# Kernel tuning notes

Hardware: AMD Instinct MI355X
Metric: run time of the kernel (lower is better)

## Reference

```python
import jax, jax.numpy as jnp
import numpy as np

B, S, H, N_HEAD = 2, 2048, 1024, 16
NEG = float(-(2 ** 32) + 1)  # -4294967295.0, the module's padding value
EPS = 1e-08


def setup_inputs() -> dict:
    key = jax.random.key(0)
    ks = jax.random.split(key, 11)
    sc = 0.02
    return {
        "queries": jax.random.normal(ks[0], (B, S, H), dtype=jnp.float32),
        "keys": jax.random.normal(ks[1], (B, S, H), dtype=jnp.float32),
        "values": jax.random.normal(ks[2], (B, S, H), dtype=jnp.float32),
        "Wq": jax.random.normal(ks[3], (H, H), dtype=jnp.float32) * sc,
        "bq": jax.random.normal(ks[4], (H,), dtype=jnp.float32) * sc,
        "Wk": jax.random.normal(ks[5], (H, H), dtype=jnp.float32) * sc,
        "bk": jax.random.normal(ks[6], (H,), dtype=jnp.float32) * sc,
        "Wv": jax.random.normal(ks[7], (H, H), dtype=jnp.float32) * sc,
        "bv": jax.random.normal(ks[8], (H,), dtype=jnp.float32) * sc,
        "Wo": jax.random.normal(ks[9], (H, H), dtype=jnp.float32) * sc,
        "bo": jax.random.normal(ks[10], (H,), dtype=jnp.float32) * sc,
    }


def reference(queries, keys, values, Wq, bq, Wk, bk, Wv, bv, Wo, bo):
    n = N_HEAD
    Bb, Sq, Hh = queries.shape
    Sk = keys.shape[1]
    d = Hh // n

    # Linear + ReLU projections
    Q = jax.nn.relu(queries @ Wq + bq)  # [B,Sq,H]
    K = jax.nn.relu(keys @ Wk + bk)     # [B,Sk,H]
    V = jax.nn.relu(values @ Wv + bv)   # [B,Sk,H]

    # chunk(dim=2) + cat(dim=0) == head-major split: [n,B,S,d]
    Q_ = Q.reshape(Bb, Sq, n, d).transpose(2, 0, 1, 3)
    K_ = K.reshape(Bb, Sk, n, d).transpose(2, 0, 1, 3)
    V_ = V.reshape(Bb, Sk, n, d).transpose(2, 0, 1, 3)

    # key padding mask from full (pre-chunk) K: [B,Sk]
    key_masks = jnp.sign(jnp.abs(jnp.sum(K, axis=-1)))

    # scores: [n,B,Sq,Sk], scaled by sqrt(per-head dim)
    scores = jnp.einsum("hbqd,hbkd->hbqk", Q_, K_) / (d ** 0.5)

    # multiplicative padding-mask selection -> equivalent where()
    scores = jnp.where(key_masks[None, :, None, :] == 0.0, NEG, scores)

    # causal tril mask (masked=True)
    tril = jnp.tril(jnp.ones((Sq, Sk), dtype=scores.dtype))
    scores = jnp.where(tril[None, None] == 0.0, NEG, scores)

    attn = jax.nn.softmax(scores, axis=-1)
    out = jnp.einsum("hbqk,hbkd->hbqd", attn, V_)  # [n,B,Sq,d]

    # cat chunks back along feature dim: [B,Sq,H]
    out = out.transpose(1, 2, 0, 3).reshape(Bb, Sq, Hh)

    out = jax.nn.relu(out @ Wo + bo)
    # sublayer connection (dropout treated as identity for determinism)
    out = queries + out

    # layer norm with torch-style unbiased std, gamma=1, beta=0
    mean = out.mean(axis=-1, keepdims=True)
    std = jnp.std(out, axis=-1, ddof=1, keepdims=True)
    return (out - mean) / (std + EPS)
```

## Files before the change

kernel.cpp:

```cpp
#include <hip/hip_runtime.h>
#include <math.h>

typedef __bf16 bf16;
typedef __attribute__((ext_vector_type(8))) __bf16 bf16x8;
typedef __attribute__((ext_vector_type(4))) __bf16 bf16x4;
typedef __attribute__((ext_vector_type(4))) float f32x4;

typedef __attribute__((address_space(1))) unsigned int glb_u32;
typedef __attribute__((address_space(3))) unsigned int lds_u32;

#define NEGV (-4294967295.0f)
#define SCL2 0.18033688011112042f

__device__ __forceinline__ void async_cp16(const void* g, void* l) {
  __builtin_amdgcn_global_load_lds((glb_u32*)g, (lds_u32*)l, 16, 0, 0);
}

template <int CTRL>
__device__ __forceinline__ float dppf(float x) {
  return __builtin_bit_cast(float,
      __builtin_amdgcn_mov_dpp(__builtin_bit_cast(int, x), CTRL, 0xF, 0xF, true));
}
__device__ __forceinline__ float dpp_max16(float x) {
  x = fmaxf(x, dppf<0xB1>(x));
  x = fmaxf(x, dppf<0x4E>(x));
  x = fmaxf(x, dppf<0x141>(x));
  x = fmaxf(x, dppf<0x140>(x));
  return x;
}

__global__ __launch_bounds__(256) void wt_kernel(
    const float* __restrict__ W0, const float* __restrict__ W1,
    const float* __restrict__ W2, const float* __restrict__ W3,
    short* T0, short* T1, short* T2, short* T3) {
  __shared__ float tile[64][65];
  const float* W = blockIdx.z == 0 ? W0 : (blockIdx.z == 1 ? W1 : (blockIdx.z == 2 ? W2 : W3));
  bf16* T = (bf16*)(blockIdx.z == 0 ? T0 : (blockIdx.z == 1 ? T1 : (blockIdx.z == 2 ? T2 : T3)));
  const int k0 = blockIdx.y * 64, n0 = blockIdx.x * 64;
  const int tid = threadIdx.x;
  const int c = tid & 63, rr = tid >> 6;
#pragma unroll
  for (int i = 0; i < 16; i++) {
    int r = i * 4 + rr;
    tile[r][c] = W[(size_t)(k0 + r) * 1024 + n0 + c];
  }
  __syncthreads();
#pragma unroll
  for (int i = 0; i < 16; i++) {
    int r = i * 4 + rr;
    T[(size_t)(n0 + r) * 1024 + k0 + c] = (bf16)tile[c][r];
  }
}

__global__ __launch_bounds__(256) void qkv_gemm(
    const float* __restrict__ Xq, const float* __restrict__ Xk,
    const float* __restrict__ Xv,
    const short* Wtq_, const short* Wtk_, const short* Wtv_,
    const float* __restrict__ bq_, const float* __restrict__ bk_, const float* __restrict__ bv_,
    short* Qo_, short* Ko_, short* Vto_) {
  __shared__ float Af[128][32];
  __shared__ bf16 Blds[128][32];
  const int which = blockIdx.z;
  const float* X = which == 0 ? Xq : (which == 1 ? Xk : Xv);
  const bf16* Wt = (const bf16*)(which == 0 ? Wtq_ : (which == 1 ? Wtk_ : Wtv_));
  const float* bias = which == 0 ? bq_ : (which == 1 ? bk_ : bv_);
  const int m0 = blockIdx.y * 128, n0 = blockIdx.x * 128;
  const int tid = threadIdx.x, wid = tid >> 6, lane = tid & 63;
  const int wr = wid >> 1, wc = wid & 1;
  const int l15 = lane & 15, lg = lane >> 4;
  const f32x4 vzero = {0.f, 0.f, 0.f, 0.f};
  f32x4 acc[4][4];
#pragma unroll
  for (int m = 0; m < 4; m++)
#pragma unroll
    for (int n = 0; n < 4; n++) acc[m][n] = vzero;

  const int asrow = lane >> 3;
  const int acbs = ((lane & 7) * 16) ^ ((asrow & 7) << 4);
  const int bsr = wid * 32 + (lane >> 2);
  const int bscb = (lane & 3) * 16;

  for (int kt = 0; kt < 32; ++kt) {
#pragma unroll
    for (int c = 0; c < 4; c++) {
      const char* ga = (const char*)(X + (size_t)(m0 + wid * 32 + c * 8 + asrow) * 1024 + kt * 32) + acbs;
      async_cp16(ga, &Af[wid * 32 + c * 8][0]);
    }
    const char* gb = (const char*)(Wt + (size_t)(n0 + bsr) * 1024 + kt * 32) + bscb;
    async_cp16(gb, &Blds[wid * 32][0]);
    async_cp16(gb + 16 * 2048, &Blds[wid * 32 + 16][0]);
    __syncthreads();
    bf16x8 a[4], bb[4];
#pragma unroll
    for (int m = 0; m < 4; m++) {
      const int row = wr * 64 + m * 16 + l15;
      const int swz = (row & 7) << 4;
      const char* ar = (const char*)&Af[0][0] + row * 128;
      const float4 f0 = *(const float4*)(ar + ((lg * 32) ^ swz));
      const float4 f1 = *(const float4*)(ar + ((lg * 32 + 16) ^ swz));
      a[m][0] = (bf16)f0.x; a[m][1] = (bf16)f0.y; a[m][2] = (bf16)f0.z; a[m][3] = (bf16)f0.w;
      a[m][4] = (bf16)f1.x; a[m][5] = (bf16)f1.y; a[m][6] = (bf16)f1.z; a[m][7] = (bf16)f1.w;
    }
#pragma unroll
    for (int n = 0; n < 4; n++) bb[n] = *(const bf16x8*)&Blds[wc * 64 + n * 16 + l15][lg * 8];
#pragma unroll
    for (int m = 0; m < 4; m++)
#pragma unroll
      for (int n = 0; n < 4; n++)
        acc[m][n] = __builtin_amdgcn_mfma_f32_16x16x32_bf16(a[m], bb[n], acc[m][n], 0, 0, 0);
    __syncthreads();
  }

  if (which != 2) {
    bf16* Y = (bf16*)(which == 0 ? Qo_ : Ko_);
    const float osc = (which == 0) ? SCL2 : 1.0f;
#pragma unroll
    for (int n = 0; n < 4; n++) {
      const int col = n0 + wc * 64 + n * 16 + l15;
      const float bv = bias[col];
#pragma unroll
      for (int m = 0; m < 4; m++) {
        const int row0 = m0 + wr * 64 + m * 16 + lg * 4;
#pragma unroll
        for (int r = 0; r < 4; r++) {
          float v = acc[m][n][r] + bv;
          v = v > 0.f ? v : 0.f;
          Y[(size_t)(row0 + r) * 1024 + col] = (bf16)(v * osc);
        }
      }
    }
  } else {
    bf16* Vt = (bf16*)Vto_;
#pragma unroll
    for (int n = 0; n < 4; n++) {
      const int col = n0 + wc * 64 + n * 16 + l15;
      const float bv = bias[col];
#pragma unroll
      for (int m = 0; m < 4; m++) {
        const int row0 = m0 + wr * 64 + m * 16 + lg * 4;
        const int bb2 = row0 >> 11;
        const int s2 = row0 & 2047;
        bf16x4 pk;
#pragma unroll
        for (int r = 0; r < 4; r++) {
          float v = acc[m][n][r] + bv;
          v = v > 0.f ? v : 0.f;
          pk[r] = (bf16)v;
        }
        *(bf16x4*)(Vt + ((size_t)bb2 * 1024 + col) * 2048 + s2) = pk;
      }
    }
  }
}

__global__ __launch_bounds__(256) void out_gemm(
    const short* A_, const short* Wt_, const float* __restrict__ bias,
    short* __restrict__ Y_) {
  __shared__ bf16 Alds[128][32];
  __shared__ bf16 Blds[128][32];
  const bf16* X = (const bf16*)A_;
  const bf16* Wt = (const bf16*)Wt_;
  bf16* Y = (bf16*)Y_;
  const int m0 = blockIdx.y * 128, n0 = blockIdx.x * 128;
  const int tid = threadIdx.x, wid = tid >> 6, lane = tid & 63;
  const int wr = wid >> 1, wc = wid & 1;
  const int l15 = lane & 15, lg = lane >> 4;
  const f32x4 vzero = {0.f, 0.f, 0.f, 0.f};
  f32x4 acc[4][4];
#pragma unroll
  for (int m = 0; m < 4; m++)
#pragma unroll
    for (int n = 0; n < 4; n++) acc[m][n] = vzero;

  const int sr = wid * 32 + (lane >> 2);
  const int scb = (lane & 3) * 16;

  for (int kt = 0; kt < 32; ++kt) {
    const char* ga = (const char*)(X + (size_t)(m0 + sr) * 1024 + kt * 32) + scb;
    async_cp16(ga, &Alds[wid * 32][0]);
    async_cp16(ga + 16 * 2048, &Alds[wid * 32 + 16][0]);
    const char* gb = (const char*)(Wt + (size_t)(n0 + sr) * 1024 + kt * 32) + scb;
    async_cp16(gb, &Blds[wid * 32][0]);
    async_cp16(gb + 16 * 2048, &Blds[wid * 32 + 16][0]);
    __syncthreads();
    bf16x8 a[4], bb[4];
#pragma unroll
    for (int m = 0; m < 4; m++) a[m] = *(const bf16x8*)&Alds[wr * 64 + m * 16 + l15][lg * 8];
#pragma unroll
    for (int n = 0; n < 4; n++) bb[n] = *(const bf16x8*)&Blds[wc * 64 + n * 16 + l15][lg * 8];
#pragma unroll
    for (int m = 0; m < 4; m++)
#pragma unroll
      for (int n = 0; n < 4; n++)
        acc[m][n] = __builtin_amdgcn_mfma_f32_16x16x32_bf16(a[m], bb[n], acc[m][n], 0, 0, 0);
    __syncthreads();
  }
#pragma unroll
  for (int n = 0; n < 4; n++) {
    const int col = n0 + wc * 64 + n * 16 + l15;
    const float bv = bias[col];
#pragma unroll
    for (int m = 0; m < 4; m++) {
      const int row0 = m0 + wr * 64 + m * 16 + lg * 4;
#pragma unroll
      for (int r = 0; r < 4; r++) {
        float v = acc[m][n][r] + bv;
        Y[(size_t)(row0 + r) * 1024 + col] = (bf16)(v > 0.f ? v : 0.f);
      }
    }
  }
}

__global__ __launch_bounds__(256) void key_mask_kernel(const short* Kb_,
                                                       unsigned* __restrict__ kbits) {
  __shared__ unsigned bits[4];
  const bf16* Kb = (const bf16*)Kb_;
  const int wid = threadIdx.x >> 6, lane = threadIdx.x & 63;
  const int row0 = blockIdx.x * 32 + wid * 8;
  unsigned mybits = 0;
#pragma unroll
  for (int i = 0; i < 8; i++) {
    const bf16x8* p = (const bf16x8*)(Kb + (size_t)(row0 + i) * 1024);
    bf16x8 v0 = p[lane];
    bf16x8 v1 = p[64 + lane];
    float s = 0.f;
#pragma unroll
    for (int jj = 0; jj < 8; jj++) s += (float)v0[jj] + (float)v1[jj];
    for (int m = 32; m; m >>= 1) s += __shfl_xor(s, m);
    if (s != 0.f) mybits |= 1u << (wid * 8 + i);
  }
  if (lane == 0) bits[wid] = mybits;
  __syncthreads();
  if (threadIdx.x == 0) kbits[blockIdx.x] = bits[0] | bits[1] | bits[2] | bits[3];
}

__device__ __forceinline__ bf16x8 lds_read_swz(const bf16* base, int row, int cbyte) {
  return *(const bf16x8*)((const char*)base + row * 128 + (cbyte ^ ((row & 7) << 4)));
}

__global__ __launch_bounds__(128) void attn_kernel(
    const short* Q_, const short* K_, const short* Vt_,
    const unsigned* __restrict__ kbits, short* O_) {
  __shared__ bf16 Klds[2][64][64];
  __shared__ bf16 Vlds[2][64][64];
  __shared__ bf16 Plds[2][16][64];
  const bf16* Q = (const bf16*)Q_;
  const bf16* K = (const bf16*)K_;
  const bf16* Vt = (const bf16*)Vt_;
  bf16* O = (bf16*)O_;

  const int f = blockIdx.x;
  const int xcd = f & 7, idx = f >> 3;
  const int qtb = idx & 31;
  const int hb = xcd + 8 * (idx >> 5);
  const int h = hb & 15, b = hb >> 4;

  const int tid = threadIdx.x, wid = tid >> 6, lane = tid & 63;
  const int l15 = lane & 15, lg = lane >> 4;
  const f32x4 vzero = {0.f, 0.f, 0.f, 0.f};
  bf16* const pbase = &Plds[wid][0][0];

  const int srow = lane >> 3;
  const int cb = (lane & 7) * 16;
  const int cbs = cb ^ ((srow & 7) << 4);

  bf16x8 vones;
#pragma unroll
  for (int i = 0; i < 8; i++) vones[i] = (bf16)1.0f;

  for (int seg = 0; seg < 2; ++seg) {
    const int qt = (seg == 0) ? qtb : 63 - qtb;
    const int q0 = qt * 32;
    const int nkt = (32 * qt + 95) >> 6;

    const int qrow = q0 + wid * 16 + l15;
    const bf16* qp = Q + ((size_t)b * 2048 + qrow) * 1024 + h * 64;
    const bf16x8 qf0 = *(const bf16x8*)(qp + lg * 8);
    const bf16x8 qf1 = *(const bf16x8*)(qp + 32 + lg * 8);

    float Mrow[4];
    f32x4 oacc[4], oaccL;
#pragma unroll
    for (int r = 0; r < 4; r++) Mrow[r] = -INFINITY;
#pragma unroll
    for (int n = 0; n < 4; n++) oacc[n] = vzero;
    oaccL = vzero;
    float Mmin = -INFINITY;

    const char* kn = (const char*)(K + ((size_t)b * 2048 + wid * 32 + srow) * 1024 + h * 64) + cbs;
    const char* vn = (const char*)(Vt + ((size_t)b * 1024 + h * 64 + wid * 32 + srow) * 2048) + cbs;

    auto STAGE = [&](int buf) {
#pragma unroll
      for (int c = 0; c < 4; c++) {
        async_cp16(kn + c * 16384, &Klds[buf][wid * 32 + c * 8][0]);
        async_cp16(vn + c * 32768, &Vlds[buf][wid * 32 + c * 8][0]);
      }
      kn += 131072;
      vn += 128;
    };

    STAGE(0);
    __syncthreads();
    int cur = 0;
    for (int kt = 0; kt < nkt; ++kt) {
      if (kt + 1 < nkt) STAGE(cur ^ 1);

      f32x4 sacc[4];
#pragma unroll
      for (int n = 0; n < 4; n++) sacc[n] = vzero;
      {
        bf16x8 kf[4];
#pragma unroll
        for (int n = 0; n < 4; n++)
          kf[n] = lds_read_swz(&Klds[cur][0][0], n * 16 + l15, lg * 16);
        __builtin_amdgcn_s_setprio(1);
#pragma unroll
        for (int n = 0; n < 4; n++)
          sacc[n] = __builtin_amdgcn_mfma_f32_16x16x32_bf16(qf0, kf[n], sacc[n], 0, 0, 0);
        __builtin_amdgcn_s_setprio(0);
#pragma unroll
        for (int n = 0; n < 4; n++)
          kf[n] = lds_read_swz(&Klds[cur][0][0], n * 16 + l15, 64 + lg * 16);
        __builtin_amdgcn_s_setprio(1);
#pragma unroll
        for (int n = 0; n < 4; n++)
          sacc[n] = __builtin_amdgcn_mfma_f32_16x16x32_bf16(qf1, kf[n], sacc[n], 0, 0, 0);
        __builtin_amdgcn_s_setprio(0);
      }

      const unsigned w0 = kbits[b * 64 + kt * 2];
      const unsigned w1 = kbits[b * 64 + kt * 2 + 1];
      const bool last = (kt == nkt - 1);
      if (last || ((w0 & w1) != 0xFFFFFFFFu)) {
        const int qrow0 = q0 + wid * 16 + lg * 4;
#pragma unroll
        for (int n = 0; n < 4; n++) {
          const unsigned wsel = (n < 2) ? w0 : w1;
          const bool on = (wsel >> ((n & 1) * 16 + l15)) & 1;
          const int kcol = kt * 64 + n * 16 + l15;
#pragma unroll
          for (int r = 0; r < 4; r++) {
            float sc = sacc[n][r];
            if (!on) sc = NEGV;
            if (last && kcol > qrow0 + r) sc = NEGV;
            sacc[n][r] = sc;
          }
        }
      }

      {
        float lm = sacc[0][0];
#pragma unroll
        for (int n = 0; n < 4; n++)
#pragma unroll
          for (int r = 0; r < 4; r++) lm = fmaxf(lm, sacc[n][r]);
        const float gmax = dpp_max16(lm);
        if (!__all(gmax <= Mmin + 8.f)) {
#pragma unroll
          for (int r = 0; r < 4; r++) {
            float tm = fmaxf(fmaxf(sacc[0][r], sacc[1][r]), fmaxf(sacc[2][r], sacc[3][r]));
            tm = dpp_max16(tm);
            const float Mn = fmaxf(Mrow[r], tm);
            const float sc = exp2f(Mrow[r] - Mn);
            Mrow[r] = Mn;
#pragma unroll
            for (int n = 0; n < 4; n++) oacc[n][r] *= sc;
            oaccL[r] *= sc;
          }
          Mmin = fminf(fminf(Mrow[0], Mrow[1]), fminf(Mrow[2], Mrow[3]));
        }
      }

#pragma unroll
      for (int n = 0; n < 4; n++)
#pragma unroll
        for (int r = 0; r < 4; r++) {
          const float p = exp2f(sacc[n][r] - Mrow[r]);
          const int prow = lg * 4 + r;
          *(bf16*)((char*)pbase + prow * 128 +
                   (((n * 16 + l15) * 2) ^ ((prow & 7) << 4))) = (bf16)p;
        }

#pragma unroll
      for (int ks = 0; ks < 2; ks++) {
        bf16x8 vf[4];
#pragma unroll
        for (int nd = 0; nd < 4; nd++)
          vf[nd] = lds_read_swz(&Vlds[cur][0][0], nd * 16 + l15, ks * 64 + lg * 16);
        const bf16x8 pf = lds_read_swz(pbase, l15, ks * 64 + lg * 16);
        __builtin_amdgcn_s_setprio(1);
#pragma unroll
        for (int nd = 0; nd < 4; nd++)
          oacc[nd] = __builtin_amdgcn_mfma_f32_16x16x32_bf16(pf, vf[nd], oacc[nd], 0, 0, 0);
        oaccL = __builtin_amdgcn_mfma_f32_16x16x32_bf16(pf, vones, oaccL, 0, 0, 0);
        __builtin_amdgcn_s_setprio(0);
      }

      __syncthreads();
      cur ^= 1;
    }

    float inv[4];
#pragma unroll
    for (int r = 0; r < 4; r++) inv[r] = 1.0f / oaccL[r];
#pragma unroll
    for (int nd = 0; nd < 4; nd++) {
      const int col = h * 64 + nd * 16 + l15;
#pragma unroll
      for (int r = 0; r < 4; r++) {
        const float v = oacc[nd][r] * inv[r];
        O[((size_t)b * 2048 + q0 + wid * 16 + lg * 4 + r) * 1024 + col] = (bf16)v;
      }
    }
  }
}

__global__ __launch_bounds__(256) void ln_kernel(const float* __restrict__ qin,
                                                 const short* __restrict__ proj_,
                                                 float* __restrict__ out) {
  __shared__ float sbuf[4];
  const bf16* proj = (const bf16*)proj_;
  const int row = blockIdx.x, tid = threadIdx.x;
  const size_t base = (size_t)row * 1024 + tid * 4;
  const float4 a = *(const float4*)(qin + base);
  const bf16x4 pb = *(const bf16x4*)(proj + base);
  const float x0 = a.x + (float)pb[0], x1 = a.y + (float)pb[1];
  const float x2 = a.z + (float)pb[2], x3 = a.w + (float)pb[3];
  float s = x0 + x1 + x2 + x3;
  for (int m = 32; m; m >>= 1) s += __shfl_xor(s, m);
  if ((tid & 63) == 0) sbuf[tid >> 6] = s;
  __syncthreads();
  s = sbuf[0] + sbuf[1] + sbuf[2] + sbuf[3];
  const float mean = s * (1.f / 1024.f);
  const float d0 = x0 - mean, d1 = x1 - mean, d2 = x2 - mean, d3 = x3 - mean;
  float ss = d0 * d0 + d1 * d1 + d2 * d2 + d3 * d3;
  __syncthreads();
  for (int m = 32; m; m >>= 1) ss += __shfl_xor(ss, m);
  if ((tid & 63) == 0) sbuf[tid >> 6] = ss;
  __syncthreads();
  ss = sbuf[0] + sbuf[1] + sbuf[2] + sbuf[3];
  const float inv = 1.f / (sqrtf(ss * (1.f / 1023.f)) + 1e-8f);
  float4 o;
  o.x = d0 * inv; o.y = d1 * inv; o.z = d2 * inv; o.w = d3 * inv;
  *(float4*)(out + base) = o;
}

extern "C" void kernel_launch(void* const* d_in, const int* in_sizes, int n_in,
                              void* d_out, int out_size, void* d_ws, size_t ws_size,
                              hipStream_t stream) {
  (void)in_sizes; (void)n_in; (void)out_size; (void)ws_size;
  const float* queries = (const float*)d_in[0];
  const float* keys    = (const float*)d_in[1];
  const float* values  = (const float*)d_in[2];
  const float* Wq = (const float*)d_in[3];  const float* bq = (const float*)d_in[4];
  const float* Wk = (const float*)d_in[5];  const float* bk = (const float*)d_in[6];
  const float* Wv = (const float*)d_in[7];  const float* bv = (const float*)d_in[8];
  const float* Wo = (const float*)d_in[9];  const float* bo = (const float*)d_in[10];
  float* out = (float*)d_out;

  char* w = (char*)d_ws;
  const size_t SZ_X = (size_t)4096 * 1024 * 2;
  const size_t SZ_W = (size_t)1024 * 1024 * 2;
  short* Wtq = (short*)w; w += SZ_W;
  short* Wtk = (short*)w; w += SZ_W;
  short* Wtv = (short*)w; w += SZ_W;
  short* Wto = (short*)w; w += SZ_W;
  short* Qb  = (short*)w; w += SZ_X;
  short* Kb  = (short*)w; w += SZ_X;
  short* Vtb = (short*)w; w += SZ_X;
  short* Ab  = (short*)w; w += SZ_X;
  short* proj = (short*)w; w += SZ_X;
  unsigned* kbits = (unsigned*)w; w += 4096;

  wt_kernel<<<dim3(16, 16, 4), 256, 0, stream>>>(Wq, Wk, Wv, Wo, Wtq, Wtk, Wtv, Wto);
  qkv_gemm<<<dim3(8, 32, 3), 256, 0, stream>>>(queries, keys, values,
                                               Wtq, Wtk, Wtv,
                                               bq, bk, bv, Qb, Kb, Vtb);
  key_mask_kernel<<<128, 256, 0, stream>>>(Kb, kbits);
  attn_kernel<<<1024, 128, 0, stream>>>(Qb, Kb, Vtb, kbits, Ab);
  out_gemm<<<dim3(8, 32), 256, 0, stream>>>(Ab, Wto, bo, proj);
  ln_kernel<<<4096, 256, 0, stream>>>(queries, proj, out);
}
```

Measured before the change: 166.0 us.

## Pre-convert QKV inputs to bf16 and swizzle bf16 LDS tiles in GEMMs

Adds a separate kernel that converts the three fp32 activation inputs to bf16 before the QKV projection. The GEMM then streams half the bytes per A tile and no longer converts fp32 to bf16 inside its inner loop. Both GEMMs now use an XOR-swizzled 64-byte-row LDS layout to reduce bank conflicts on the fragment reads. The cost is an extra launch plus a full read and write pass over 48 MB of fp32 input, and more workspace.

```diff
diff --git a/kernel.cpp b/kernel.cpp
--- a/kernel.cpp
+++ b/kernel.cpp
@@ -27,6 +27,20 @@
   x = fmaxf(x, dppf<0x141>(x));
   x = fmaxf(x, dppf<0x140>(x));
   return x;
+}
+
+__global__ __launch_bounds__(256) void cvt3_kernel(
+    const float* __restrict__ q, const float* __restrict__ k,
+    const float* __restrict__ v, short* xq, short* xk, short* xv) {
+  const int bid = blockIdx.x;
+  const int which = bid >> 12;
+  const int i = (bid & 4095) * 256 + threadIdx.x;
+  const float* src = which == 0 ? q : (which == 1 ? k : v);
+  short* dst = which == 0 ? xq : (which == 1 ? xk : xv);
+  float4 vv = ((const float4*)src)[i];
+  bf16x4 o;
+  o[0] = (bf16)vv.x; o[1] = (bf16)vv.y; o[2] = (bf16)vv.z; o[3] = (bf16)vv.w;
+  ((bf16x4*)dst)[i] = o;
 }
 
 __global__ __launch_bounds__(256) void wt_kernel(
@@ -52,16 +66,19 @@
   }
 }
 
+__device__ __forceinline__ bf16x8 lds_read_swz64(const bf16* base, int row, int cbyte) {
+  return *(const bf16x8*)((const char*)base + row * 64 + (cbyte ^ (((row >> 1) & 3) << 4)));
+}
+
 __global__ __launch_bounds__(256) void qkv_gemm(
-    const float* __restrict__ Xq, const float* __restrict__ Xk,
-    const float* __restrict__ Xv,
+    const short* Xq_, const short* Xk_, const short* Xv_,
     const short* Wtq_, const short* Wtk_, const short* Wtv_,
     const float* __restrict__ bq_, const float* __restrict__ bk_, const float* __restrict__ bv_,
     short* Qo_, short* Ko_, short* Vto_) {
-  __shared__ float Af[128][32];
+  __shared__ bf16 Alds[128][32];
   __shared__ bf16 Blds[128][32];
   const int which = blockIdx.z;
-  const float* X = which == 0 ? Xq : (which == 1 ? Xk : Xv);
+  const bf16* X  = (const bf16*)(which == 0 ? Xq_  : (which == 1 ? Xk_  : Xv_));
   const bf16* Wt = (const bf16*)(which == 0 ? Wtq_ : (which == 1 ? Wtk_ : Wtv_));
   const float* bias = which == 0 ? bq_ : (which == 1 ? bk_ : bv_);
   const int m0 = blockIdx.y * 128, n0 = blockIdx.x * 128;
@@ -75,34 +92,23 @@
 #pragma unroll
     for (int n = 0; n < 4; n++) acc[m][n] = vzero;
 
-  const int asrow = lane >> 3;
-  const int acbs = ((lane & 7) * 16) ^ ((asrow & 7) << 4);
-  const int bsr = wid * 32 + (lane >> 2);
-  const int bscb = (lane & 3) * 16;
+  const int srow = lane >> 2;
+  const int scbs = ((lane & 3) * 16) ^ (((srow >> 1) & 3) << 4);
 
   for (int kt = 0; kt < 32; ++kt) {
 #pragma unroll
-    for (int c = 0; c < 4; c++) {
-      const char* ga = (const char*)(X + (size_t)(m0 + wid * 32 + c * 8 + asrow) * 1024 + kt * 32) + acbs;
-      async_cp16(ga, &Af[wid * 32 + c * 8][0]);
-    }
-    const char* gb = (const char*)(Wt + (size_t)(n0 + bsr) * 1024 + kt * 32) + bscb;
-    async_cp16(gb, &Blds[wid * 32][0]);
-    async_cp16(gb + 16 * 2048, &Blds[wid * 32 + 16][0]);
+    for (int c = 0; c < 2; c++) {
+      const char* ga = (const char*)(X + (size_t)(m0 + wid * 32 + c * 16 + srow) * 1024 + kt * 32) + scbs;
+      async_cp16(ga, &Alds[wid * 32 + c * 16][0]);
+      const char* gb = (const char*)(Wt + (size_t)(n0 + wid * 32 + c * 16 + srow) * 1024 + kt * 32) + scbs;
+      async_cp16(gb, &Blds[wid * 32 + c * 16][0]);
+    }
     __syncthreads();
     bf16x8 a[4], bb[4];
 #pragma unroll
-    for (int m = 0; m < 4; m++) {
-      const int row = wr * 64 + m * 16 + l15;
-      const int swz = (row & 7) << 4;
-      const char* ar = (const char*)&Af[0][0] + row * 128;
-      const float4 f0 = *(const float4*)(ar + ((lg * 32) ^ swz));
-      const float4 f1 = *(const float4*)(ar + ((lg * 32 + 16) ^ swz));
-      a[m][0] = (bf16)f0.x; a[m][1] = (bf16)f0.y; a[m][2] = (bf16)f0.z; a[m][3] = (bf16)f0.w;
-      a[m][4] = (bf16)f1.x; a[m][5] = (bf16)f1.y; a[m][6] = (bf16)f1.z; a[m][7] = (bf16)f1.w;
-    }
-#pragma unroll
-    for (int n = 0; n < 4; n++) bb[n] = *(const bf16x8*)&Blds[wc * 64 + n * 16 + l15][lg * 8];
+    for (int m = 0; m < 4; m++) a[m] = lds_read_swz64(&Alds[0][0], wr * 64 + m * 16 + l15, lg * 16);
+#pragma unroll
+    for (int n = 0; n < 4; n++) bb[n] = lds_read_swz64(&Blds[0][0], wc * 64 + n * 16 + l15, lg * 16);
 #pragma unroll
     for (int m = 0; m < 4; m++)
 #pragma unroll
@@ -172,22 +178,23 @@
 #pragma unroll
     for (int n = 0; n < 4; n++) acc[m][n] = vzero;
 
-  const int sr = wid * 32 + (lane >> 2);
-  const int scb = (lane & 3) * 16;
+  const int srow = lane >> 2;
+  const int scbs = ((lane & 3) * 16) ^ (((srow >> 1) & 3) << 4);
 
   for (int kt = 0; kt < 32; ++kt) {
-    const char* ga = (const char*)(X + (size_t)(m0 + sr) * 1024 + kt * 32) + scb;
-    async_cp16(ga, &Alds[wid * 32][0]);
-    async_cp16(ga + 16 * 2048, &Alds[wid * 32 + 16][0]);
-    const char* gb = (const char*)(Wt + (size_t)(n0 + sr) * 1024 + kt * 32) + scb;
-    async_cp16(gb, &Blds[wid * 32][0]);
-    async_cp16(gb + 16 * 2048, &Blds[wid * 32 + 16][0]);
+#pragma unroll
+    for (int c = 0; c < 2; c++) {
+      const char* ga = (const char*)(X + (size_t)(m0 + wid * 32 + c * 16 + srow) * 1024 + kt * 32) + scbs;
+      async_cp16(ga, &Alds[wid * 32 + c * 16][0]);
+      const char* gb = (const char*)(Wt + (size_t)(n0 + wid * 32 + c * 16 + srow) * 1024 + kt * 32) + scbs;
+      async_cp16(gb, &Blds[wid * 32 + c * 16][0]);
+    }
     __syncthreads();
     bf16x8 a[4], bb[4];
 #pragma unroll
-    for (int m = 0; m < 4; m++) a[m] = *(const bf16x8*)&Alds[wr * 64 + m * 16 + l15][lg * 8];
-#pragma unroll
-    for (int n = 0; n < 4; n++) bb[n] = *(const bf16x8*)&Blds[wc * 64 + n * 16 + l15][lg * 8];
+    for (int m = 0; m < 4; m++) a[m] = lds_read_swz64(&Alds[0][0], wr * 64 + m * 16 + l15, lg * 16);
+#pragma unroll
+    for (int n = 0; n < 4; n++) bb[n] = lds_read_swz64(&Blds[0][0], wc * 64 + n * 16 + l15, lg * 16);
 #pragma unroll
     for (int m = 0; m < 4; m++)
 #pragma unroll
@@ -462,6 +469,9 @@
   char* w = (char*)d_ws;
   const size_t SZ_X = (size_t)4096 * 1024 * 2;
   const size_t SZ_W = (size_t)1024 * 1024 * 2;
+  short* Xq  = (short*)w; w += SZ_X;
+  short* Xk  = (short*)w; w += SZ_X;
+  short* Xv  = (short*)w; w += SZ_X;
   short* Wtq = (short*)w; w += SZ_W;
   short* Wtk = (short*)w; w += SZ_W;
   short* Wtv = (short*)w; w += SZ_W;
@@ -473,9 +483,9 @@
   short* proj = (short*)w; w += SZ_X;
   unsigned* kbits = (unsigned*)w; w += 4096;
 
+  cvt3_kernel<<<12288, 256, 0, stream>>>(queries, keys, values, Xq, Xk, Xv);
   wt_kernel<<<dim3(16, 16, 4), 256, 0, stream>>>(Wq, Wk, Wv, Wo, Wtq, Wtk, Wtv, Wto);
-  qkv_gemm<<<dim3(8, 32, 3), 256, 0, stream>>>(queries, keys, values,
-                                               Wtq, Wtk, Wtv,
+  qkv_gemm<<<dim3(8, 32, 3), 256, 0, stream>>>(Xq, Xk, Xv, Wtq, Wtk, Wtv,
                                                bq, bk, bv, Qb, Kb, Vtb);
   key_mask_kernel<<<128, 256, 0, stream>>>(Kb, kbits);
   attn_kernel<<<1024, 128, 0, stream>>>(Qb, Kb, Vtb, kbits, Ab);
```

Result: faster. 149.1 us (-10.2%).
